# Optimization experiments

Hardware: AMD Instinct MI355X
Metric: run time of the kernel (lower is better)

Reference implementation:

```python
import jax, jax.numpy as jnp
import numpy as np

B = 512          # batch == number of memories
S = 8            # num_attention_splits
U = 512          # num_units = sum(num_units_regions)
D = 32           # dim_attention_unit
G = 8            # num_attention_groups
MASK_P = 0.1
DIM_IN = 4096
DAG = 2048       # dim_attention_global


def setup_inputs() -> dict:
    key = jax.random.key(0)
    ks = jax.random.split(key, 8)
    # xavier-normal-ish scales for the unit-wise linears
    s1 = (2.0 / (DIM_IN // S + DAG // S)) ** 0.5
    s2 = (2.0 / (DAG // S + U * D // S)) ** 0.5
    return {
        "x": jax.random.normal(ks[0], (B, DIM_IN), jnp.float32),
        "mem_attention": jax.random.normal(ks[1], (B, U, D), jnp.float32),
        "mem_outputs": jax.random.normal(ks[2], (B, U, D), jnp.float32),
        "rand_u": jax.random.uniform(ks[3], (B, B, U), jnp.float32),
        "w1": jax.random.normal(ks[4], (S, DIM_IN // S, DAG // S), jnp.float32) * s1,
        "b1": jnp.zeros((S, DAG // S), jnp.float32),
        "w2": jax.random.normal(ks[5], (S, DAG // S, U * D // S), jnp.float32) * s2,
        "b2": jnp.zeros((S, U * D // S), jnp.float32),
        "temperature": jnp.ones((U,), jnp.float32),
    }


def reference(x, mem_attention, mem_outputs, rand_u, w1, b1, w2, b2, temperature):
    # attentions(): split input, two unit-wise linears
    xs = x.reshape(B, S, DIM_IN // S)                        # [B,S,I/S]
    ga = jnp.einsum("bsi,sio->bso", xs, w1) + b1             # [B,S,DAG/S]
    att = jnp.einsum("bso,soj->bsj", ga, w2) + b2            # [B,S,U*D/S]
    att = att.reshape(B, U, D)                               # [B,U,D]
    ga_flat = ga.reshape(B, DAG)                             # [B,DAG]

    # per-unit pairwise scores: (att_b . mem_att_m) per unit  -> [B,M,U]
    weights = jnp.einsum("bud,mud->bmu", att, mem_attention)
    weights = weights * temperature                          # broadcast over U

    neg_inf = jnp.float32(-jnp.inf)
    weights = jnp.where(rand_u < MASK_P, neg_inf, weights)   # random mask
    eye = jnp.eye(B, dtype=bool)[:, :, None]                 # self-exclusion
    weights = jnp.where(eye, neg_inf, weights)

    # group-wise softmax over the memory axis
    w = weights.reshape(B, B // G, G, U)
    w = jax.nn.softmax(w, axis=1)
    w = w.reshape(B, B, U) / 8.0

    # weighted reduction over memories (avoids [B,B,U,D] intermediate)
    outputs = jnp.einsum("bmu,mud->bud", w, mem_outputs)     # [B,U,D]
    return att, ga_flat, w, outputs
```

## Files before the change

kernel.cpp:

```cpp
#include <hip/hip_runtime.h>
#include <math.h>

#define NEGBIG (-1e30f)


__global__ __launch_bounds__(256) void gemm_split(
    const float* __restrict__ A, int lda, int Ksz,
    const float* __restrict__ Bw, int NS,
    const float* __restrict__ bias,
    float* __restrict__ C, int ldc)
{
  const int n0 = blockIdx.x * 64;
  const int b0 = blockIdx.y * 64;
  const int s  = n0 / NS;
  const float* Bp = Bw + (size_t)s * Ksz * NS;
  const int nloc0 = n0 - s * NS;
  const int acol0 = s * Ksz;

  __shared__ float As[16][64];
  __shared__ float Bs[16][64];

  const int t  = threadIdx.x;
  const int tb = t & 15, tn = t >> 4;
  float acc[4][4] = {};

  for (int k0 = 0; k0 < Ksz; k0 += 16) {
    {
      int r = t & 63, g = t >> 6;
      float4 v = *reinterpret_cast<const float4*>(
          A + (size_t)(b0 + r) * lda + acol0 + k0 + 4 * g);
      As[4*g+0][r] = v.x; As[4*g+1][r] = v.y; As[4*g+2][r] = v.z; As[4*g+3][r] = v.w;
    }
    {
      int kk = t >> 4, n4 = t & 15;
      float4 v = *reinterpret_cast<const float4*>(
          Bp + (size_t)(k0 + kk) * NS + nloc0 + 4 * n4);
      *reinterpret_cast<float4*>(&Bs[kk][4*n4]) = v;
    }
    __syncthreads();
#pragma unroll
    for (int k = 0; k < 16; ++k) {
      float4 a4 = *reinterpret_cast<const float4*>(&As[k][4*tb]);
      float4 b4 = *reinterpret_cast<const float4*>(&Bs[k][4*tn]);
      float av[4] = {a4.x, a4.y, a4.z, a4.w};
      float bv[4] = {b4.x, b4.y, b4.z, b4.w};
#pragma unroll
      for (int i = 0; i < 4; ++i)
#pragma unroll
        for (int j = 0; j < 4; ++j)
          acc[i][j] = fmaf(av[i], bv[j], acc[i][j]);
    }
    __syncthreads();
  }
#pragma unroll
  for (int i = 0; i < 4; ++i) {
    int row = b0 + 4*tb + i;
    int col = n0 + 4*tn;
    float4 o;
    o.x = acc[i][0] + bias[col + 0];
    o.y = acc[i][1] + bias[col + 1];
    o.z = acc[i][2] + bias[col + 2];
    o.w = acc[i][3] + bias[col + 3];
    *reinterpret_cast<float4*>(C + (size_t)row * ldc + col) = o;
  }
}

__global__ __launch_bounds__(256) void scores_psum_kernel(
    const float* __restrict__ att,
    const float* __restrict__ ma,
    const float* __restrict__ rnd,
    const float* __restrict__ temp,
    float* __restrict__ wout,
    float* __restrict__ stats)
{
  __shared__ float At[16 * 516];
  __shared__ float Ma[16 * 260];
  const int b0 = blockIdx.x * 16;
  const int u0 = blockIdx.y * 16;
  const int t  = threadIdx.x;
  const int u  = t & 15, tb = (t >> 4) & 3, tm = t >> 6;

  {
    int r = t >> 4, base = t & 15;
    const float* src = att + (size_t)(b0 + r) * 16384 + u0 * 32;
#pragma unroll
    for (int g = 0; g < 8; ++g) {
      int i4 = base + 16 * g;
      int uu = i4 >> 3, d4 = i4 & 7;
      float4 v = *reinterpret_cast<const float4*>(src + 4 * i4);
      *reinterpret_cast<float4*>(&At[uu*516 + d4*64 + (r ^ ((2*d4) & 15))*4]) = v;
    }
  }
  const float tmp = temp[u0 + u];
  float Ls[4][2];
#pragma unroll
  for (int i = 0; i < 4; ++i)
#pragma unroll
    for (int j = 0; j < 2; ++j) Ls[i][j] = 0.f;

  for (int m0 = 0; m0 < 512; m0 += 8) {
    float rv[4][2];
#pragma unroll
    for (int i = 0; i < 4; ++i)
#pragma unroll
      for (int j = 0; j < 2; ++j)
        rv[i][j] = rnd[((size_t)(b0 + 4*tb + i) * 512 + m0 + 2*tm + j) * 512 + u0 + u];
    __syncthreads();
    {
      int r = t >> 5, base = t & 31;
      const float* src = ma + (size_t)(m0 + r) * 16384 + u0 * 32;
#pragma unroll
      for (int g = 0; g < 4; ++g) {
        int i4 = base + 32 * g;
        int uu = i4 >> 3, d4 = i4 & 7;
        float4 v = *reinterpret_cast<const float4*>(src + 4 * i4);
        *reinterpret_cast<float4*>(&Ma[uu*260 + d4*32 + ((r ^ d4) & 7)*4]) = v;
      }
    }
    __syncthreads();
    float acc[4][2] = {};
#pragma unroll
    for (int d4 = 0; d4 < 8; ++d4) {
      const int sw = (2*d4) & 15;
      float4 av[4], mv[2];
#pragma unroll
      for (int i = 0; i < 4; ++i)
        av[i] = *reinterpret_cast<const float4*>(&At[u*516 + d4*64 + ((4*tb+i) ^ sw)*4]);
#pragma unroll
      for (int j = 0; j < 2; ++j)
        mv[j] = *reinterpret_cast<const float4*>(&Ma[u*260 + d4*32 + (((2*tm+j) ^ d4) & 7)*4]);
#pragma unroll
      for (int i = 0; i < 4; ++i)
#pragma unroll
        for (int j = 0; j < 2; ++j) {
          acc[i][j] = fmaf(av[i].x, mv[j].x, acc[i][j]);
          acc[i][j] = fmaf(av[i].y, mv[j].y, acc[i][j]);
          acc[i][j] = fmaf(av[i].z, mv[j].z, acc[i][j]);
          acc[i][j] = fmaf(av[i].w, mv[j].w, acc[i][j]);
        }
    }
#pragma unroll
    for (int i = 0; i < 4; ++i)
#pragma unroll
      for (int j = 0; j < 2; ++j) {
        int gb = b0 + 4*tb + i, gm = m0 + 2*tm + j;
        float p;
        if ((rv[i][j] < 0.1f) | (gm == gb)) p = 0.f;
        else                                p = __expf(acc[i][j] * tmp);
        wout[((size_t)gb * 512 + gm) * 512 + u0 + u] = p;
        Ls[i][j] += p;
      }
  }
#pragma unroll
  for (int i = 0; i < 4; ++i)
#pragma unroll
    for (int j = 0; j < 2; ++j) {
      int b = b0 + 4*tb + i, g = 2*tm + j;
      stats[((size_t)b * 512 + u0 + u) * 32 + g] = 1.0f / (8.0f * Ls[i][j]);
    }
}

__global__ __launch_bounds__(256) void emit_outputs_v3(
    const float* __restrict__ mo,
    float* __restrict__ w,
    float* __restrict__ outs)
{
  __shared__ float MoL[8 * 16 * 32];
  __shared__ float E[8 * 16 * 17];
  const int u0 = blockIdx.x * 16;
  const int b0 = blockIdx.y * 16;
  const int t  = threadIdx.x;
  const int ab = t >> 4, am = (t >> 1) & 7, uh = t & 1;
  const int pu = t >> 4, bq = (t >> 2) & 3, dh = t & 3;

  float Sreg[8];
  {
    const float* cb = outs + ((size_t)(b0 + ab) * 512 + u0 + uh * 8) * 32;
#pragma unroll
    for (int j = 0; j < 8; ++j) Sreg[j] = cb[j * 32 + am];
  }

  float4 acc[4][2];
#pragma unroll
  for (int i = 0; i < 4; ++i) {
    acc[i][0] = make_float4(0.f, 0.f, 0.f, 0.f);
    acc[i][1] = make_float4(0.f, 0.f, 0.f, 0.f);
  }

  float* wbase = w + (size_t)(b0 + ab) * 262144 + u0 + uh * 8;

  const float* msrc0;  const float* msrc1;  const float* msrc2;  const float* msrc3;
  int loff0, loff1, loff2, loff3;
  {
    int P, mm, uu, dq;
    P = t;          mm = P >> 7; uu = (P >> 3) & 15; dq = P & 7;
    msrc0 = mo + (size_t)mm * 16384 + (size_t)(u0 + uu) * 32 + (dq ^ (uu & 7)) * 4;
    loff0 = P * 4;
    P = 256 + t;    mm = P >> 7; uu = (P >> 3) & 15; dq = P & 7;
    msrc1 = mo + (size_t)mm * 16384 + (size_t)(u0 + uu) * 32 + (dq ^ (uu & 7)) * 4;
    loff1 = P * 4;
    P = 512 + t;    mm = P >> 7; uu = (P >> 3) & 15; dq = P & 7;
    msrc2 = mo + (size_t)mm * 16384 + (size_t)(u0 + uu) * 32 + (dq ^ (uu & 7)) * 4;
    loff2 = P * 4;
    P = 768 + t;    mm = P >> 7; uu = (P >> 3) & 15; dq = P & 7;
    msrc3 = mo + (size_t)mm * 16384 + (size_t)(u0 + uu) * 32 + (dq ^ (uu & 7)) * 4;
    loff3 = P * 4;
  }

  float4 wpre0, wpre1, smo0, smo1, smo2, smo3;
  {
    const float* wp = wbase + (size_t)am * 512;
    wpre0 = *reinterpret_cast<const float4*>(wp);
    wpre1 = *reinterpret_cast<const float4*>(wp + 4);
    smo0 = *reinterpret_cast<const float4*>(msrc0);
    smo1 = *reinterpret_cast<const float4*>(msrc1);
    smo2 = *reinterpret_cast<const float4*>(msrc2);
    smo3 = *reinterpret_cast<const float4*>(msrc3);
  }

#pragma unroll 1
  for (int c = 0; c < 64; ++c) {
    const int mc = c * 8;
    if (c) __syncthreads();

    {
      float* wp = wbase + (size_t)(mc + am) * 512;
      float s0[4] = {wpre0.x, wpre0.y, wpre0.z, wpre0.w};
      float s1[4] = {wpre1.x, wpre1.y, wpre1.z, wpre1.w};
#pragma unroll
      for (int e2 = 0; e2 < 4; ++e2) {
        float v = s0[e2] * Sreg[e2];
        s0[e2] = v;
        E[(am * 16 + uh * 8 + e2) * 17 + ab] = v;
      }
#pragma unroll
      for (int e2 = 0; e2 < 4; ++e2) {
        float v = s1[e2] * Sreg[4 + e2];
        s1[e2] = v;
        E[(am * 16 + uh * 8 + 4 + e2) * 17 + ab] = v;
      }
      *reinterpret_cast<float4*>(wp)     = make_float4(s0[0], s0[1], s0[2], s0[3]);
      *reinterpret_cast<float4*>(wp + 4) = make_float4(s1[0], s1[1], s1[2], s1[3]);
    }
    *reinterpret_cast<float4*>(&MoL[loff0]) = smo0;
    *reinterpret_cast<float4*>(&MoL[loff1]) = smo1;
    *reinterpret_cast<float4*>(&MoL[loff2]) = smo2;
    *reinterpret_cast<float4*>(&MoL[loff3]) = smo3;
    __syncthreads();

    if (c < 63) {
      const float* wp = wbase + (size_t)(mc + 8 + am) * 512;
      wpre0 = *reinterpret_cast<const float4*>(wp);
      wpre1 = *reinterpret_cast<const float4*>(wp + 4);
      const size_t moff = (size_t)(mc + 8) * 16384;
      smo0 = *reinterpret_cast<const float4*>(msrc0 + moff);
      smo1 = *reinterpret_cast<const float4*>(msrc1 + moff);
      smo2 = *reinterpret_cast<const float4*>(msrc2 + moff);
      smo3 = *reinterpret_cast<const float4*>(msrc3 + moff);
    }

#pragma unroll
    for (int m = 0; m < 8; ++m) {
      float4 ef = *reinterpret_cast<const float4*>(&E[(m * 16 + pu) * 17 + 4 * bq]);
      float4 v0 = *reinterpret_cast<const float4*>(
          &MoL[(m * 16 + pu) * 32 + (((2 * dh) ^ (pu & 7)) * 4)]);
      float4 v1 = *reinterpret_cast<const float4*>(
          &MoL[(m * 16 + pu) * 32 + (((2 * dh + 1) ^ (pu & 7)) * 4)]);
      float es[4] = {ef.x, ef.y, ef.z, ef.w};
#pragma unroll
      for (int i = 0; i < 4; ++i) {
        acc[i][0].x = fmaf(es[i], v0.x, acc[i][0].x);
        acc[i][0].y = fmaf(es[i], v0.y, acc[i][0].y);
        acc[i][0].z = fmaf(es[i], v0.z, acc[i][0].z);
        acc[i][0].w = fmaf(es[i], v0.w, acc[i][0].w);
        acc[i][1].x = fmaf(es[i], v1.x, acc[i][1].x);
        acc[i][1].y = fmaf(es[i], v1.y, acc[i][1].y);
        acc[i][1].z = fmaf(es[i], v1.z, acc[i][1].z);
        acc[i][1].w = fmaf(es[i], v1.w, acc[i][1].w);
      }
    }
  }

#pragma unroll
  for (int i = 0; i < 4; ++i) {
    float* dst = outs + ((size_t)(b0 + 4 * bq + i) * 512 + u0 + pu) * 32 + 8 * dh;
    *reinterpret_cast<float4*>(dst)     = acc[i][0];
    *reinterpret_cast<float4*>(dst + 4) = acc[i][1];
  }
}

extern "C" void kernel_launch(void* const* d_in, const int* in_sizes, int n_in,
                              void* d_out, int out_size, void* d_ws, size_t ws_size,
                              hipStream_t stream) {
  const float* x    = (const float*)d_in[0];
  const float* ma   = (const float*)d_in[1];
  const float* mo   = (const float*)d_in[2];
  const float* rnd  = (const float*)d_in[3];
  const float* w1   = (const float*)d_in[4];
  const float* b1   = (const float*)d_in[5];
  const float* w2   = (const float*)d_in[6];
  const float* b2   = (const float*)d_in[7];
  const float* temp = (const float*)d_in[8];

  float* out  = (float*)d_out;
  float* att  = out;
  float* ga   = out + 8388608;
  float* wbuf = out + 9437184;
  float* outs = out + 143654912;

  gemm_split<<<dim3(32, 8), 256, 0, stream>>>(x, 4096, 512, w1, 256, b1, ga, 2048);
  gemm_split<<<dim3(256, 8), 256, 0, stream>>>(ga, 2048, 256, w2, 2048, b2, att, 16384);
  scores_psum_kernel<<<dim3(32, 32), 256, 0, stream>>>(att, ma, rnd, temp, wbuf, outs);
  emit_outputs_v3<<<dim3(32, 32), 256, 0, stream>>>(mo, wbuf, outs);
}
```

Measured before the change: 900.2 us.

## Rewrite scores kernel with register-resident att, async LDS loads, and prefetch

```diff
diff --git a/kernel.cpp b/kernel.cpp
--- a/kernel.cpp
+++ b/kernel.cpp
@@ -2,6 +2,8 @@
 #include <math.h>
 
 #define NEGBIG (-1e30f)
+#define GLB_PTR(x) ((const __attribute__((address_space(1))) void*)(x))
+#define LDS_PTR(x) ((__attribute__((address_space(3))) void*)(x))
 
 
 __global__ __launch_bounds__(256) void gemm_split(
@@ -65,7 +67,7 @@
   }
 }
 
-__global__ __launch_bounds__(256) void scores_psum_kernel(
+__global__ __launch_bounds__(256) void scores_psum_v3(
     const float* __restrict__ att,
     const float* __restrict__ ma,
     const float* __restrict__ rnd,
@@ -73,91 +75,135 @@
     float* __restrict__ wout,
     float* __restrict__ stats)
 {
-  __shared__ float At[16 * 516];
-  __shared__ float Ma[16 * 260];
+  __shared__ float MaL[16 * 16 * 32];
   const int b0 = blockIdx.x * 16;
   const int u0 = blockIdx.y * 16;
   const int t  = threadIdx.x;
-  const int u  = t & 15, tb = (t >> 4) & 3, tm = t >> 6;
-
-  {
-    int r = t >> 4, base = t & 15;
-    const float* src = att + (size_t)(b0 + r) * 16384 + u0 * 32;
-#pragma unroll
-    for (int g = 0; g < 8; ++g) {
-      int i4 = base + 16 * g;
-      int uu = i4 >> 3, d4 = i4 & 7;
-      float4 v = *reinterpret_cast<const float4*>(src + 4 * i4);
-      *reinterpret_cast<float4*>(&At[uu*516 + d4*64 + (r ^ ((2*d4) & 15))*4]) = v;
-    }
+  const int u = t & 15, tbb = (t >> 4) & 7, tm = t >> 7;
+  const int w = t >> 6, l = t & 63;
+
+  float4 A[2][8];
+#pragma unroll
+  for (int i = 0; i < 2; ++i) {
+    const float* ap = att + (size_t)(b0 + 2 * tbb + i) * 16384
+                    + (size_t)(u0 + u) * 32;
+#pragma unroll
+    for (int k = 0; k < 8; ++k)
+      A[i][k] = *reinterpret_cast<const float4*>(ap + 4 * k);
   }
   const float tmp = temp[u0 + u];
-  float Ls[4][2];
-#pragma unroll
-  for (int i = 0; i < 4; ++i)
-#pragma unroll
-    for (int j = 0; j < 2; ++j) Ls[i][j] = 0.f;
-
-  for (int m0 = 0; m0 < 512; m0 += 8) {
-    float rv[4][2];
-#pragma unroll
-    for (int i = 0; i < 4; ++i)
-#pragma unroll
-      for (int j = 0; j < 2; ++j)
-        rv[i][j] = rnd[((size_t)(b0 + 4*tb + i) * 512 + m0 + 2*tm + j) * 512 + u0 + u];
-    __syncthreads();
-    {
-      int r = t >> 5, base = t & 31;
-      const float* src = ma + (size_t)(m0 + r) * 16384 + u0 * 32;
-#pragma unroll
-      for (int g = 0; g < 4; ++g) {
-        int i4 = base + 32 * g;
-        int uu = i4 >> 3, d4 = i4 & 7;
-        float4 v = *reinterpret_cast<const float4*>(src + 4 * i4);
-        *reinterpret_cast<float4*>(&Ma[uu*260 + d4*32 + ((r ^ d4) & 7)*4]) = v;
-      }
-    }
-    __syncthreads();
-    float acc[4][2] = {};
+
+  int offK[8];
+#pragma unroll
+  for (int k = 0; k < 8; ++k) {
+    int slot = (w * 8 + k) * 64 + l;
+    int mm = slot >> 7, uu = (slot >> 3) & 15, dqS = slot & 7;
+    offK[k] = mm * 16384 + (u0 + uu) * 32 + ((dqS ^ (uu & 7)) << 2);
+  }
+
+  const float* rrow0 = rnd + (size_t)(b0 + 2 * tbb) * 262144 + u0 + u;
+  const float* rrow1 = rrow0 + 262144;
+  float* wrow0 = wout + (size_t)(b0 + 2 * tbb) * 262144 + u0 + u;
+  float* wrow1 = wrow0 + 262144;
+
+  float Ls[2][8];
+#pragma unroll
+  for (int i = 0; i < 2; ++i)
+#pragma unroll
+    for (int j = 0; j < 8; ++j) Ls[i][j] = 0.f;
+
+#pragma unroll
+  for (int k = 0; k < 8; ++k)
+    __builtin_amdgcn_global_load_lds(GLB_PTR(ma + (size_t)offK[k]),
+                                     LDS_PTR(&MaL[(w * 8 + k) * 256]), 16, 0, 0);
+  float rc[2][8], rn[2][8];
+#pragma unroll
+  for (int j = 0; j < 8; ++j) {
+    rc[0][j] = rrow0[(size_t)(8 * tm + j) * 512];
+    rc[1][j] = rrow1[(size_t)(8 * tm + j) * 512];
+  }
+
+#pragma unroll 1
+  for (int c = 0; c < 32; ++c) {
+    const int m0 = c * 16;
+    __syncthreads();
+
+    if (c < 31) {
+#pragma unroll
+      for (int j = 0; j < 8; ++j) {
+        rn[0][j] = rrow0[(size_t)(m0 + 16 + 8 * tm + j) * 512];
+        rn[1][j] = rrow1[(size_t)(m0 + 16 + 8 * tm + j) * 512];
+      }
+    }
+
+    float acc[2][8] = {};
 #pragma unroll
     for (int d4 = 0; d4 < 8; ++d4) {
-      const int sw = (2*d4) & 15;
-      float4 av[4], mv[2];
-#pragma unroll
-      for (int i = 0; i < 4; ++i)
-        av[i] = *reinterpret_cast<const float4*>(&At[u*516 + d4*64 + ((4*tb+i) ^ sw)*4]);
-#pragma unroll
-      for (int j = 0; j < 2; ++j)
-        mv[j] = *reinterpret_cast<const float4*>(&Ma[u*260 + d4*32 + (((2*tm+j) ^ d4) & 7)*4]);
-#pragma unroll
-      for (int i = 0; i < 4; ++i)
-#pragma unroll
-        for (int j = 0; j < 2; ++j) {
-          acc[i][j] = fmaf(av[i].x, mv[j].x, acc[i][j]);
-          acc[i][j] = fmaf(av[i].y, mv[j].y, acc[i][j]);
-          acc[i][j] = fmaf(av[i].z, mv[j].z, acc[i][j]);
-          acc[i][j] = fmaf(av[i].w, mv[j].w, acc[i][j]);
-        }
-    }
-#pragma unroll
-    for (int i = 0; i < 4; ++i)
-#pragma unroll
-      for (int j = 0; j < 2; ++j) {
-        int gb = b0 + 4*tb + i, gm = m0 + 2*tm + j;
-        float p;
-        if ((rv[i][j] < 0.1f) | (gm == gb)) p = 0.f;
-        else                                p = __expf(acc[i][j] * tmp);
-        wout[((size_t)gb * 512 + gm) * 512 + u0 + u] = p;
-        Ls[i][j] += p;
-      }
-  }
-#pragma unroll
-  for (int i = 0; i < 4; ++i)
-#pragma unroll
-    for (int j = 0; j < 2; ++j) {
-      int b = b0 + 4*tb + i, g = 2*tm + j;
-      stats[((size_t)b * 512 + u0 + u) * 32 + g] = 1.0f / (8.0f * Ls[i][j]);
-    }
+      const int dsw = d4 ^ (u & 7);
+      const float4 a0 = A[0][d4], a1 = A[1][d4];
+#pragma unroll
+      for (int j = 0; j < 8; ++j) {
+        float4 mv = *reinterpret_cast<const float4*>(
+            &MaL[(((8 * tm + j) * 128) + u * 8 + dsw) * 4]);
+        acc[0][j] = fmaf(a0.x, mv.x, acc[0][j]);
+        acc[0][j] = fmaf(a0.y, mv.y, acc[0][j]);
+        acc[0][j] = fmaf(a0.z, mv.z, acc[0][j]);
+        acc[0][j] = fmaf(a0.w, mv.w, acc[0][j]);
+        acc[1][j] = fmaf(a1.x, mv.x, acc[1][j]);
+        acc[1][j] = fmaf(a1.y, mv.y, acc[1][j]);
+        acc[1][j] = fmaf(a1.z, mv.z, acc[1][j]);
+        acc[1][j] = fmaf(a1.w, mv.w, acc[1][j]);
+      }
+    }
+
+#pragma unroll
+    for (int j = 0; j < 8; ++j) {
+      const int gm = m0 + 8 * tm + j;
+      {
+        const int gb = b0 + 2 * tbb;
+        float p = ((rc[0][j] < 0.1f) | (gm == gb)) ? 0.f
+                                                   : __expf(acc[0][j] * tmp);
+        wrow0[(size_t)gm * 512] = p;
+        Ls[0][j] += p;
+      }
+      {
+        const int gb = b0 + 2 * tbb + 1;
+        float p = ((rc[1][j] < 0.1f) | (gm == gb)) ? 0.f
+                                                   : __expf(acc[1][j] * tmp);
+        wrow1[(size_t)gm * 512] = p;
+        Ls[1][j] += p;
+      }
+    }
+
+    __syncthreads();
+    if (c < 31) {
+#pragma unroll
+      for (int k = 0; k < 8; ++k)
+        __builtin_amdgcn_global_load_lds(
+            GLB_PTR(ma + (size_t)offK[k] + (size_t)(m0 + 16) * 16384),
+            LDS_PTR(&MaL[(w * 8 + k) * 256]), 16, 0, 0);
+#pragma unroll
+      for (int j = 0; j < 8; ++j) { rc[0][j] = rn[0][j]; rc[1][j] = rn[1][j]; }
+    }
+  }
+
+  __syncthreads();
+#pragma unroll
+  for (int i = 0; i < 2; ++i)
+#pragma unroll
+    for (int j = 0; j < 8; ++j)
+      MaL[t * 16 + i * 8 + j] = Ls[i][j];
+  __syncthreads();
+  if (tm == 0) {
+#pragma unroll
+    for (int i = 0; i < 2; ++i)
+#pragma unroll
+      for (int j = 0; j < 8; ++j) {
+        float tot = Ls[i][j] + MaL[(t + 128) * 16 + i * 8 + j];
+        stats[((size_t)(b0 + 2 * tbb + i) * 512 + u0 + u) * 32 + j] =
+            1.0f / (8.0f * tot);
+      }
+  }
 }
 
 __global__ __launch_bounds__(256) void emit_outputs_v3(
@@ -310,6 +356,6 @@
 
   gemm_split<<<dim3(32, 8), 256, 0, stream>>>(x, 4096, 512, w1, 256, b1, ga, 2048);
   gemm_split<<<dim3(256, 8), 256, 0, stream>>>(ga, 2048, 256, w2, 2048, b2, att, 16384);
-  scores_psum_kernel<<<dim3(32, 32), 256, 0, stream>>>(att, ma, rnd, temp, wbuf, outs);
+  scores_psum_v3<<<dim3(32, 32), 256, 0, stream>>>(att, ma, rnd, temp, wbuf, outs);
   emit_outputs_v3<<<dim3(32, 32), 256, 0, stream>>>(mo, wbuf, outs);
 }
```

Measured after the change: 843.2 us. -6.3%, faster.
